# Performance work log

Hardware: AMD Instinct MI355X
Metric: run time of the kernel (lower is better)

The kernel has to match this reference:

```python
import jax, jax.numpy as jnp
import numpy as np

TAU = 2.0      # spikingjelly LIF default membrane time constant
VTH = 1.0      # threshold
SCALE = 0.25
NUM_HEADS = 16
EPS = 1e-5


def lif(x):
    # single-step LIF from rest (v=0, v_reset=0): u = v + (x - v)/tau = x/tau; spike = H(u - vth)
    return (x / TAU >= VTH).astype(x.dtype)


def bn(z, gamma, beta, mean, var):
    # inference-mode BatchNorm1d over channel dim of (TB, C, N)
    inv = gamma / jnp.sqrt(var + EPS)
    return z * inv[:, None] + (beta - mean * inv)[:, None]


def branch(z, w, gamma, beta, mean, var):
    # conv1x1 (pointwise channel mix) -> BN -> LIF
    z = jnp.einsum('oc,bcn->bon', w, z)
    return lif(bn(z, gamma, beta, mean, var))


def setup_inputs() -> dict:
    key = jax.random.key(0)
    ks = jax.random.split(key, 8)
    T, B, C, N = 4, 2, 512, 512
    x = jax.random.normal(ks[0], (T, B, C, N), dtype=jnp.float32)
    y = jax.random.normal(ks[1], (T, B, C, N), dtype=jnp.float32)
    def conv_w(k):
        return jax.random.normal(k, (C, C), dtype=jnp.float32) / np.float32(np.sqrt(C))
    def bn_params(k):
        km, kv = jax.random.split(k)
        gamma = jnp.full((C,), 2.0, dtype=jnp.float32)  # scale so LIF spikes are non-trivially sparse
        beta = jnp.zeros((C,), dtype=jnp.float32)
        mean = 0.1 * jax.random.normal(km, (C,), dtype=jnp.float32)
        var = 0.5 + jax.random.uniform(kv, (C,), dtype=jnp.float32)
        return gamma, beta, mean, var
    q_g, q_b, q_m, q_v = bn_params(ks[2])
    k_g, k_b, k_m, k_v = bn_params(ks[3])
    v_g, v_b, v_m, v_v = bn_params(ks[4])
    p_g, p_b, p_m, p_v = bn_params(ks[5])
    return {
        'x': x, 'y': y,
        'q_w': conv_w(jax.random.fold_in(key, 10)), 'q_g': q_g, 'q_b': q_b, 'q_m': q_m, 'q_v': q_v,
        'k_w': conv_w(jax.random.fold_in(key, 11)), 'k_g': k_g, 'k_b': k_b, 'k_m': k_m, 'k_v': k_v,
        'v_w': conv_w(jax.random.fold_in(key, 12)), 'v_g': v_g, 'v_b': v_b, 'v_m': v_m, 'v_v': v_v,
        'p_w': conv_w(jax.random.fold_in(key, 13)), 'p_g': p_g, 'p_b': p_b, 'p_m': p_m, 'p_v': p_v,
    }


def reference(x, y, q_w, q_g, q_b, q_m, q_v, k_w, k_g, k_b, k_m, k_v,
              v_w, v_g, v_b, v_m, v_v, p_w, p_g, p_b, p_m, p_v):
    T, B, C, N = x.shape
    H = NUM_HEADS
    D = C // H
    xq = x.reshape(T * B, C, N)
    yk = y.reshape(T * B, C, N)
    # q/k/v: conv1x1 + BN + LIF, then split heads: (T,B,C,N) -> (T,B,H,N,D)
    q = branch(xq, q_w, q_g, q_b, q_m, q_v).reshape(T, B, H, D, N).transpose(0, 1, 2, 4, 3)
    k = branch(yk, k_w, k_g, k_b, k_m, k_v).reshape(T, B, H, D, N).transpose(0, 1, 2, 4, 3)
    v = branch(yk, v_w, v_g, v_b, v_m, v_v).reshape(T, B, H, D, N).transpose(0, 1, 2, 4, 3)
    # softmax-free spiking attention: (Q K^T) V * scale
    attn = jnp.einsum('tbhnd,tbhmd->tbhnm', q, k)
    o = jnp.einsum('tbhnm,tbhmd->tbhnd', attn, v) * SCALE
    o = o.transpose(0, 1, 2, 4, 3).reshape(T, B, C, N)  # (T,B,H,D,N) -> (T,B,C,N)
    o = lif(o.reshape(T * B, C, N))
    o = branch(o, p_w, p_g, p_b, p_m, p_v).reshape(T, B, C, N)
    return o
```

## Files before the change

kernel.cpp:

```cpp
#include <hip/hip_runtime.h>
#include <math.h>

#define TBD 8
#define CD  512
#define ND  512
#define PLANE (TBD*CD*ND)
#define WPL   (CD*CD)

typedef unsigned short u16;
typedef unsigned int u32;
typedef _Float16 f16;
typedef __attribute__((ext_vector_type(8))) short bf16x8;
typedef __attribute__((ext_vector_type(8))) _Float16 f16x8;
typedef __attribute__((ext_vector_type(4))) float f32x4;

__device__ __forceinline__ float b2f(u16 u){
  union{u32 i; float f;} x; x.i = ((u32)u) << 16; return x.f;
}
__device__ __forceinline__ u16 f2b(float f){
  u32 u = __builtin_bit_cast(u32, f);
  u += 0x7fffu + ((u >> 16) & 1u);
  return (u16)(u >> 16);
}
__device__ __forceinline__ void async_ld16(const void* g, void* l){
  __builtin_amdgcn_global_load_lds((const __attribute__((address_space(1))) u32*)g,
      (__attribute__((address_space(3))) u32*)l, 16, 0, 0);
}

__global__ __launch_bounds__(256) void prep(
    const float* __restrict__ x, const float* __restrict__ y,
    const float* __restrict__ Qw, const float* __restrict__ Kw,
    const float* __restrict__ Vw, const float* __restrict__ Pw,
    const float* __restrict__ Qg, const float* __restrict__ Qb, const float* __restrict__ Qm, const float* __restrict__ Qv,
    const float* __restrict__ Kg, const float* __restrict__ Kb, const float* __restrict__ Km, const float* __restrict__ Kv,
    const float* __restrict__ Vg, const float* __restrict__ Vb, const float* __restrict__ Vm, const float* __restrict__ Vv,
    const float* __restrict__ Pg, const float* __restrict__ Pb, const float* __restrict__ Pm, const float* __restrict__ Pv,
    u16* __restrict__ wsu, float* __restrict__ ib)
{
  const int bx = blockIdx.x, t = threadIdx.x;
  if (bx < 1024) {
    __shared__ __align__(16) float tl[64][68];
    const int inp = bx >> 9, rem = bx & 511;
    const int tb = rem >> 6, tile = rem & 63;
    const int ct = (tile & 7) << 6, nt = (tile >> 3) << 6;
    const float* xg = inp ? y : x;
    #pragma unroll
    for (int r = 0; r < 4; ++r) {
      const int row = (t >> 4) + (r << 4);
      const int col = (t & 15) << 2;
      *(float4*)&tl[row][col] =
          *(const float4*)(xg + ((size_t)(tb*CD + ct + row))*ND + nt + col);
    }
    __syncthreads();
    const int nl = t >> 2, cb = (t & 3) << 4;
    __align__(16) u16 h[3][16];
    #pragma unroll
    for (int j = 0; j < 16; ++j) {
      const float f = tl[cb + j][nl];
      const u16 a = f2b(f);  const float r1 = f - b2f(a);
      const u16 b = f2b(r1); const float r2 = r1 - b2f(b);
      h[0][j] = a; h[1][j] = b; h[2][j] = f2b(r2);
    }
    u16* base = wsu + (size_t)inp*3*PLANE;
    const size_t rowo = ((size_t)tb*ND + nt + nl)*CD + ct + cb;
    #pragma unroll
    for (int s = 0; s < 3; ++s) {
      *(uint4*)(base + (size_t)s*PLANE + rowo)     = *(uint4*)&h[s][0];
      *(uint4*)(base + (size_t)s*PLANE + rowo + 8) = *(uint4*)&h[s][8];
    }
  } else if (bx < 2048) {
    const int b2 = bx - 1024;
    const int mat = b2 >> 8, rr = b2 & 255;
    const float* Wg = (mat==0)?Qw:(mat==1)?Kw:(mat==2)?Vw:Pw;
    const int row = (rr << 1) + (t >> 7);
    const int col = (t & 127) << 2;
    const float4 w = *(const float4*)(Wg + (size_t)row*CD + col);
    const float f[4] = {w.x, w.y, w.z, w.w};
    __align__(8) u16 h[3][4];
    #pragma unroll
    for (int j = 0; j < 4; ++j) {
      const u16 a = f2b(f[j]);  const float r1 = f[j] - b2f(a);
      const u16 b = f2b(r1);    const float r2 = r1 - b2f(b);
      h[0][j] = a; h[1][j] = b; h[2][j] = f2b(r2);
    }
    u16* base = wsu + (size_t)6*PLANE + (size_t)mat*3*WPL;
    #pragma unroll
    for (int s = 0; s < 3; ++s)
      *(uint2*)(base + (size_t)s*WPL + (size_t)row*CD + col) = *(uint2*)&h[s][0];
  } else {
    const int idx = (bx - 2048)*256 + t;
    const int br = idx >> 9, ch = idx & 511;
    const float* G = (br==0)?Qg:(br==1)?Kg:(br==2)?Vg:Pg;
    const float* B = (br==0)?Qb:(br==1)?Kb:(br==2)?Vb:Pb;
    const float* M = (br==0)?Qm:(br==1)?Km:(br==2)?Vm:Pm;
    const float* V = (br==0)?Qv:(br==1)?Kv:(br==2)?Vv:Pv;
    const float inv = G[ch] / sqrtf(V[ch] + 1e-5f);
    ib[br*1024 + ch]       = inv;
    ib[br*1024 + 512 + ch] = B[ch] - M[ch]*inv;
  }
}

template<int XS>
__global__ __launch_bounds__(256) void gemm_mfma(
    const u16* __restrict__ Ab, const u16* __restrict__ Bbp,
    const float* __restrict__ ibp,
    u16* __restrict__ spk, float* __restrict__ outf)
{
  const int bx  = blockIdx.x;
  const int idx = bx & 511;
  const int br  = bx >> 9;
  const int tb  = idx & 7;
  const int o0  = ((idx >> 3) & 7) << 6;
  const int n0  = (idx >> 6) << 6;
  const int t    = threadIdx.x;
  const int lane = t & 63, wave = t >> 6;

  const u16* A = Ab + (size_t)br*3*WPL;
  const u16* B = Bbp + (size_t)(br ? 3 : 0)*PLANE;
  const float* IB = ibp + br*1024;

  __shared__ __align__(16) u16 smem[2*3*4*512 + 2*XS*4*512];
  u16* Al = smem;
  u16* Bl = smem + 2*3*4*512;

  const int lr = lane >> 2;
  const int lc = ((lane & 3) ^ ((lane >> 3) & 3)) << 3;
  constexpr int TPW = (12 + 4*XS) / 4;

  auto stage = [&](int buf, int c0) {
    #pragma unroll
    for (int j = 0; j < TPW; ++j) {
      const int tix = wave*TPW + j;
      if (tix < 12) {
        const int s = tix >> 2, ot = tix & 3;
        async_ld16(A + (size_t)s*WPL + (size_t)(o0 + (ot<<4) + lr)*CD + c0 + lc,
                   Al + (((buf*3 + s)*4 + ot) << 9) + (lane << 3));
      } else {
        const int k = tix - 12, s = k >> 2, nt = k & 3;
        async_ld16(B + (size_t)s*PLANE + ((size_t)tb*ND + n0 + (nt<<4) + lr)*CD + c0 + lc,
                   Bl + (((buf*XS + s)*4 + nt) << 9) + (lane << 3));
      }
    }
  };

  f32x4 acc[2][2];
  const f32x4 zero = {0.f, 0.f, 0.f, 0.f};
  acc[0][0] = zero; acc[0][1] = zero; acc[1][0] = zero; acc[1][1] = zero;

  const int otb = (wave >> 1) << 1;
  const int ntb = (wave & 1) << 1;
  const int fo = ((lane & 15) << 5) + ((((lane >> 4) ^ ((lane >> 1) & 3)) & 3) << 3);

  stage(0, 0);
  for (int i = 0; i < 16; ++i) {
    const int buf = i & 1;
    __syncthreads();
    if (i < 15) stage(buf ^ 1, (i + 1) << 5);

    bf16x8 Af[3][2], Bf[XS][2];
    #pragma unroll
    for (int s = 0; s < 3; ++s)
      #pragma unroll
      for (int oy = 0; oy < 2; ++oy)
        Af[s][oy] = *(const bf16x8*)(Al + (((buf*3 + s)*4 + otb + oy) << 9) + fo);
    #pragma unroll
    for (int s = 0; s < XS; ++s)
      #pragma unroll
      for (int nx = 0; nx < 2; ++nx)
        Bf[s][nx] = *(const bf16x8*)(Bl + (((buf*XS + s)*4 + ntb + nx) << 9) + fo);

    auto mm = [&](int sa, int sb) {
      #pragma unroll
      for (int oy = 0; oy < 2; ++oy)
        #pragma unroll
        for (int nx = 0; nx < 2; ++nx)
          acc[oy][nx] = __builtin_amdgcn_mfma_f32_16x16x32_bf16(
              Af[sa][oy], Bf[sb][nx], acc[oy][nx], 0, 0, 0);
    };
    if constexpr (XS == 3) {
      mm(0,0); mm(0,1); mm(1,0); mm(1,1); mm(0,2); mm(2,0);
    } else {
      mm(0,0); mm(1,0); mm(2,0);
    }
  }

  const int rbase = (lane >> 4) << 2;
  const int cl = lane & 15;
  #pragma unroll
  for (int oy = 0; oy < 2; ++oy) {
    #pragma unroll
    for (int r = 0; r < 4; ++r) {
      const int ch = o0 + ((otb + oy) << 4) + rbase + r;
      const float inv  = IB[ch];
      const float bias = IB[512 + ch];
      #pragma unroll
      for (int nx = 0; nx < 2; ++nx) {
        const bool sp = (acc[oy][nx][r] * inv + bias >= 2.0f);
        const int n = n0 + ((ntb + nx) << 4) + cl;
        const size_t off = ((size_t)tb*CD + ch)*ND + n;
        if constexpr (XS == 1) outf[off] = sp ? 1.0f : 0.0f;
        else spk[(size_t)br*PLANE + off] = sp ? (u16)0x3C00 : (u16)0;
      }
    }
  }
}

__global__ __launch_bounds__(256) void attn(
    const u16* __restrict__ Qs, const u16* __restrict__ Ks,
    const u16* __restrict__ Vs, u16* __restrict__ S2T)
{
  const int tbh = blockIdx.x >> 2;
  const int n0  = (blockIdx.x & 3) << 7;
  const int t = threadIdx.x, lane = t & 63, wave = t >> 6;
  const int tb = tbh >> 4, h = tbh & 15;

  __shared__ __align__(16) u16 Kt[2*8*512];
  __shared__ __align__(16) u16 Vt[2*8*512];
  __shared__ __align__(16) u16 Qg[8*520];
  __shared__ __align__(16) u16 Gt[4*32*40];
  __shared__ __align__(16) u16 Sb[128*40];

  const u16* Kh = Ks + (size_t)tbh*32*ND;
  const u16* Vh = Vs + (size_t)tbh*32*ND;
  const u16* Qh = Qs + (size_t)tbh*32*ND;

  const int lr = lane >> 2;
  const int lc = ((lane & 3) ^ ((lane >> 3) & 3)) << 3;
  const int fo = ((lane & 15) << 5) + ((((lane >> 4) ^ ((lane >> 1) & 3)) & 3) << 3);

  f32x4 g[2][2];
  const f32x4 zero = {0.f, 0.f, 0.f, 0.f};
  g[0][0] = zero; g[0][1] = zero; g[1][0] = zero; g[1][1] = zero;

  for (int half = 0; half < 2; ++half) {
    if (half) __syncthreads();
    #pragma unroll
    for (int j = 0; j < 8; ++j) {
      const int u = wave*8 + j;
      const int mat = u >> 4, dt = (u >> 3) & 1, kc = u & 7;
      const u16* src = (mat ? Vh : Kh) + (size_t)((dt << 4) + lr)*ND + (half << 8) + (kc << 5) + lc;
      u16* dst = (mat ? Vt : Kt) + (((dt << 3) + kc) << 9) + (lane << 3);
      async_ld16(src, dst);
    }
    if (half == 0) {
      #pragma unroll
      for (int j = 0; j < 2; ++j) {
        const int gq = wave*2 + j;
        async_ld16(Qh + (size_t)((gq << 2) + (lane >> 4))*ND + n0 + ((lane & 15) << 3),
                   Qg + gq*520 + (lane << 3));
      }
    }
    __syncthreads();
    for (int kc = 0; kc < 8; ++kc) {
      const f16* kt = (const f16*)Kt;
      const f16* vt = (const f16*)Vt;
      f16x8 ka0 = *(const f16x8*)(kt + (kc << 9) + fo);
      f16x8 ka1 = *(const f16x8*)(kt + ((8 + kc) << 9) + fo);
      f16x8 vb0 = *(const f16x8*)(vt + (kc << 9) + fo);
      f16x8 vb1 = *(const f16x8*)(vt + ((8 + kc) << 9) + fo);
      g[0][0] = __builtin_amdgcn_mfma_f32_16x16x32_f16(ka0, vb0, g[0][0], 0,0,0);
      g[0][1] = __builtin_amdgcn_mfma_f32_16x16x32_f16(ka0, vb1, g[0][1], 0,0,0);
      g[1][0] = __builtin_amdgcn_mfma_f32_16x16x32_f16(ka1, vb0, g[1][0], 0,0,0);
      g[1][1] = __builtin_amdgcn_mfma_f32_16x16x32_f16(ka1, vb1, g[1][1], 0,0,0);
    }
  }

  f16* myG = (f16*)(Gt + wave*(32*40));
  const int rq = (lane >> 4) << 2, cl = lane & 15;
  #pragma unroll
  for (int d1t = 0; d1t < 2; ++d1t)
    #pragma unroll
    for (int d2t = 0; d2t < 2; ++d2t)
      #pragma unroll
      for (int r = 0; r < 4; ++r) {
        const int d1 = (d1t << 4) + rq + r;
        const int d2 = (d2t << 4) + cl;
        myG[d2*40 + d1] = (f16)g[d1t][d2t][r];
      }
  asm volatile("s_waitcnt lgkmcnt(0)" ::: "memory");

  f32x4 o[2][2];
  o[0][0] = zero; o[0][1] = zero; o[1][0] = zero; o[1][1] = zero;
  const f16* ql = (const f16*)Qg;
  const int kg = lane >> 4, n16 = lane & 15;
  #pragma unroll
  for (int ntl = 0; ntl < 2; ++ntl) {
    const int n0w = ((wave << 1) + ntl) << 4;
    f16x8 qb;
    #pragma unroll
    for (int j = 0; j < 8; ++j)
      qb[j] = ql[(2*kg + (j >> 2))*520 + (j & 3)*128 + n0w + n16];
    #pragma unroll
    for (int dd = 0; dd < 2; ++dd) {
      f16x8 ga = *(const f16x8*)(myG + (((dd << 4) + cl)*40) + (kg << 3));
      o[dd][ntl] = __builtin_amdgcn_mfma_f32_16x16x32_f16(ga, qb, o[dd][ntl], 0,0,0);
    }
  }

  #pragma unroll
  for (int dd = 0; dd < 2; ++dd)
    #pragma unroll
    for (int ntl = 0; ntl < 2; ++ntl)
      #pragma unroll
      for (int r = 0; r < 4; ++r) {
        const int n_local = ((wave*2 + ntl) << 4) + cl;
        const int c_local = (dd << 4) + rq + r;
        Sb[n_local*40 + c_local] = (o[dd][ntl][r] >= 8.0f) ? (u16)0x3F80 : (u16)0;
      }
  asm volatile("s_waitcnt lgkmcnt(0)" ::: "memory");

  const int nr = (wave << 5) + (lane >> 1);
  const int cs = (lane & 1) << 4;
  u16* dst = S2T + ((size_t)tb*ND + n0 + nr)*CD + (h << 5) + cs;
  *(uint4*)dst       = *(uint4*)&Sb[nr*40 + cs];
  *(uint4*)(dst + 8) = *(uint4*)&Sb[nr*40 + cs + 8];
}

extern "C" void kernel_launch(void* const* d_in, const int* in_sizes, int n_in,
                              void* d_out, int out_size, void* d_ws, size_t ws_size,
                              hipStream_t stream)
{
  const float* x  = (const float*)d_in[0];
  const float* y  = (const float*)d_in[1];
  const float* qw = (const float*)d_in[2];
  const float* qg = (const float*)d_in[3];
  const float* qb = (const float*)d_in[4];
  const float* qm = (const float*)d_in[5];
  const float* qv = (const float*)d_in[6];
  const float* kw = (const float*)d_in[7];
  const float* kg = (const float*)d_in[8];
  const float* kb = (const float*)d_in[9];
  const float* km = (const float*)d_in[10];
  const float* kv = (const float*)d_in[11];
  const float* vw = (const float*)d_in[12];
  const float* vg = (const float*)d_in[13];
  const float* vb = (const float*)d_in[14];
  const float* vm = (const float*)d_in[15];
  const float* vv = (const float*)d_in[16];
  const float* pw = (const float*)d_in[17];
  const float* pg = (const float*)d_in[18];
  const float* pb = (const float*)d_in[19];
  const float* pm = (const float*)d_in[20];
  const float* pv = (const float*)d_in[21];

  u16* wsu = (u16*)d_ws;
  u16* Wq   = wsu + (size_t)6*PLANE;
  u16* SPK  = wsu + (size_t)6*PLANE + 12*WPL;
  u16* S2T  = SPK + (size_t)3*PLANE;
  float* ib = (float*)(SPK + (size_t)4*PLANE);

  prep<<<2056, 256, 0, stream>>>(x, y, qw, kw, vw, pw,
      qg, qb, qm, qv, kg, kb, km, kv, vg, vb, vm, vv, pg, pb, pm, pv,
      wsu, ib);

  gemm_mfma<3><<<1536, 256, 0, stream>>>(Wq, wsu, ib, SPK, nullptr);

  attn<<<512, 256, 0, stream>>>(SPK, SPK + (size_t)PLANE, SPK + 2*(size_t)PLANE, S2T);

  gemm_mfma<1><<<512, 256, 0, stream>>>(Wq + (size_t)9*WPL, S2T,
      ib + 3*1024, nullptr, (float*)d_out);
}
```

Measured before the change: 170.8 us.

## Fuse K and V projections sharing Y tile; deepen K-step in output GEMM

The QKV GEMM launch now interleaves blocks. Even blocks compute Q from X, and odd blocks compute K and V together from the same staged Y tile, which halves the loads of Y for those two branches and the block count. The final projection GEMM becomes its own kernel that stages 64-wide K chunks, so it runs 8 iterations instead of 16 and needs fewer barriers. The cost is larger shared memory per block (up to 72KB), which lowers occupancy, and an unbalanced load between Q blocks and K/V blocks.

```diff
diff --git a/kernel.cpp b/kernel.cpp
--- a/kernel.cpp
+++ b/kernel.cpp
@@ -100,108 +100,186 @@
   }
 }
 
-template<int XS>
-__global__ __launch_bounds__(256) void gemm_mfma(
-    const u16* __restrict__ Ab, const u16* __restrict__ Bbp,
-    const float* __restrict__ ibp,
-    u16* __restrict__ spk, float* __restrict__ outf)
+__global__ __launch_bounds__(256) void gemm_qkv(
+    const u16* __restrict__ Wb, const u16* __restrict__ Xs,
+    const u16* __restrict__ Ys, const float* __restrict__ ib,
+    u16* __restrict__ spk)
 {
   const int bx  = blockIdx.x;
-  const int idx = bx & 511;
-  const int br  = bx >> 9;
+  const int idx = bx >> 1;
   const int tb  = idx & 7;
   const int o0  = ((idx >> 3) & 7) << 6;
   const int n0  = (idx >> 6) << 6;
   const int t    = threadIdx.x;
   const int lane = t & 63, wave = t >> 6;
 
-  const u16* A = Ab + (size_t)br*3*WPL;
-  const u16* B = Bbp + (size_t)(br ? 3 : 0)*PLANE;
-  const float* IB = ibp + br*1024;
-
-  __shared__ __align__(16) u16 smem[2*3*4*512 + 2*XS*4*512];
-  u16* Al = smem;
-  u16* Bl = smem + 2*3*4*512;
+  __shared__ __align__(16) u16 smem[2*36*512];
 
   const int lr = lane >> 2;
   const int lc = ((lane & 3) ^ ((lane >> 3) & 3)) << 3;
-  constexpr int TPW = (12 + 4*XS) / 4;
-
-  auto stage = [&](int buf, int c0) {
-    #pragma unroll
-    for (int j = 0; j < TPW; ++j) {
-      const int tix = wave*TPW + j;
-      if (tix < 12) {
-        const int s = tix >> 2, ot = tix & 3;
-        async_ld16(A + (size_t)s*WPL + (size_t)(o0 + (ot<<4) + lr)*CD + c0 + lc,
-                   Al + (((buf*3 + s)*4 + ot) << 9) + (lane << 3));
-      } else {
-        const int k = tix - 12, s = k >> 2, nt = k & 3;
-        async_ld16(B + (size_t)s*PLANE + ((size_t)tb*ND + n0 + (nt<<4) + lr)*CD + c0 + lc,
-                   Bl + (((buf*XS + s)*4 + nt) << 9) + (lane << 3));
-      }
-    }
-  };
-
-  f32x4 acc[2][2];
-  const f32x4 zero = {0.f, 0.f, 0.f, 0.f};
-  acc[0][0] = zero; acc[0][1] = zero; acc[1][0] = zero; acc[1][1] = zero;
-
   const int otb = (wave >> 1) << 1;
   const int ntb = (wave & 1) << 1;
   const int fo = ((lane & 15) << 5) + ((((lane >> 4) ^ ((lane >> 1) & 3)) & 3) << 3);
-
-  stage(0, 0);
-  for (int i = 0; i < 16; ++i) {
-    const int buf = i & 1;
-    __syncthreads();
-    if (i < 15) stage(buf ^ 1, (i + 1) << 5);
-
-    bf16x8 Af[3][2], Bf[XS][2];
-    #pragma unroll
-    for (int s = 0; s < 3; ++s)
-      #pragma unroll
-      for (int oy = 0; oy < 2; ++oy)
-        Af[s][oy] = *(const bf16x8*)(Al + (((buf*3 + s)*4 + otb + oy) << 9) + fo);
-    #pragma unroll
-    for (int s = 0; s < XS; ++s)
-      #pragma unroll
-      for (int nx = 0; nx < 2; ++nx)
-        Bf[s][nx] = *(const bf16x8*)(Bl + (((buf*XS + s)*4 + ntb + nx) << 9) + fo);
-
-    auto mm = [&](int sa, int sb) {
-      #pragma unroll
-      for (int oy = 0; oy < 2; ++oy)
-        #pragma unroll
-        for (int nx = 0; nx < 2; ++nx)
-          acc[oy][nx] = __builtin_amdgcn_mfma_f32_16x16x32_bf16(
-              Af[sa][oy], Bf[sb][nx], acc[oy][nx], 0, 0, 0);
-    };
-    if constexpr (XS == 3) {
-      mm(0,0); mm(0,1); mm(1,0); mm(1,1); mm(0,2); mm(2,0);
-    } else {
-      mm(0,0); mm(1,0); mm(2,0);
-    }
-  }
-
+  const f32x4 zero = {0.f, 0.f, 0.f, 0.f};
   const int rbase = (lane >> 4) << 2;
   const int cl = lane & 15;
-  #pragma unroll
-  for (int oy = 0; oy < 2; ++oy) {
-    #pragma unroll
-    for (int r = 0; r < 4; ++r) {
-      const int ch = o0 + ((otb + oy) << 4) + rbase + r;
-      const float inv  = IB[ch];
-      const float bias = IB[512 + ch];
-      #pragma unroll
-      for (int nx = 0; nx < 2; ++nx) {
-        const bool sp = (acc[oy][nx][r] * inv + bias >= 2.0f);
-        const int n = n0 + ((ntb + nx) << 4) + cl;
-        const size_t off = ((size_t)tb*CD + ch)*ND + n;
-        if constexpr (XS == 1) outf[off] = sp ? 1.0f : 0.0f;
-        else spk[(size_t)br*PLANE + off] = sp ? (u16)0x3C00 : (u16)0;
-      }
-    }
+
+  if (!(bx & 1)) {
+    const u16* A = Wb;
+    const u16* B = Xs;
+    const float* IB = ib;
+    u16* Al = smem;
+    u16* Bl = smem + 2*3*4*512;
+
+    auto stage = [&](int buf, int c0) {
+      #pragma unroll
+      for (int j = 0; j < 6; ++j) {
+        const int tix = wave*6 + j;
+        if (tix < 12) {
+          const int s = tix >> 2, ot = tix & 3;
+          async_ld16(A + (size_t)s*WPL + (size_t)(o0 + (ot<<4) + lr)*CD + c0 + lc,
+                     Al + (((buf*3 + s)*4 + ot) << 9) + (lane << 3));
+        } else {
+          const int k = tix - 12, s = k >> 2, nt = k & 3;
+          async_ld16(B + (size_t)s*PLANE + ((size_t)tb*ND + n0 + (nt<<4) + lr)*CD + c0 + lc,
+                     Bl + (((buf*3 + s)*4 + nt) << 9) + (lane << 3));
+        }
+      }
+    };
+
+    f32x4 acc[2][2];
+    acc[0][0] = zero; acc[0][1] = zero; acc[1][0] = zero; acc[1][1] = zero;
+
+    stage(0, 0);
+    for (int i = 0; i < 16; ++i) {
+      const int buf = i & 1;
+      __syncthreads();
+      if (i < 15) stage(buf ^ 1, (i + 1) << 5);
+
+      bf16x8 Af[3][2], Bf[3][2];
+      #pragma unroll
+      for (int s = 0; s < 3; ++s)
+        #pragma unroll
+        for (int oy = 0; oy < 2; ++oy)
+          Af[s][oy] = *(const bf16x8*)(Al + (((buf*3 + s)*4 + otb + oy) << 9) + fo);
+      #pragma unroll
+      for (int s = 0; s < 3; ++s)
+        #pragma unroll
+        for (int nx = 0; nx < 2; ++nx)
+          Bf[s][nx] = *(const bf16x8*)(Bl + (((buf*3 + s)*4 + ntb + nx) << 9) + fo);
+
+      auto mm = [&](int sa, int sb) {
+        #pragma unroll
+        for (int oy = 0; oy < 2; ++oy)
+          #pragma unroll
+          for (int nx = 0; nx < 2; ++nx)
+            acc[oy][nx] = __builtin_amdgcn_mfma_f32_16x16x32_bf16(
+                Af[sa][oy], Bf[sb][nx], acc[oy][nx], 0, 0, 0);
+      };
+      mm(0,0); mm(0,1); mm(1,0); mm(1,1); mm(0,2); mm(2,0);
+    }
+
+    #pragma unroll
+    for (int oy = 0; oy < 2; ++oy)
+      #pragma unroll
+      for (int r = 0; r < 4; ++r) {
+        const int ch = o0 + ((otb + oy) << 4) + rbase + r;
+        const float inv  = IB[ch];
+        const float bias = IB[512 + ch];
+        #pragma unroll
+        for (int nx = 0; nx < 2; ++nx) {
+          const bool sp = (acc[oy][nx][r] * inv + bias >= 2.0f);
+          const int n = n0 + ((ntb + nx) << 4) + cl;
+          spk[((size_t)tb*CD + ch)*ND + n] = sp ? (u16)0x3C00 : (u16)0;
+        }
+      }
+  } else {
+    const u16* Ak = Wb + (size_t)3*WPL;
+    const u16* Av = Wb + (size_t)6*WPL;
+    const u16* B  = Ys;
+    const float* IBk = ib + 1024;
+    const float* IBv = ib + 2048;
+
+    auto stage = [&](int buf, int c0) {
+      #pragma unroll
+      for (int j = 0; j < 9; ++j) {
+        const int tix = wave*9 + j;
+        const u16* g;
+        if (tix < 12) {
+          const int s = tix >> 2, ot = tix & 3;
+          g = Ak + (size_t)s*WPL + (size_t)(o0 + (ot<<4) + lr)*CD + c0 + lc;
+        } else if (tix < 24) {
+          const int k = tix - 12, s = k >> 2, ot = k & 3;
+          g = Av + (size_t)s*WPL + (size_t)(o0 + (ot<<4) + lr)*CD + c0 + lc;
+        } else {
+          const int k = tix - 24, s = k >> 2, nt = k & 3;
+          g = B + (size_t)s*PLANE + ((size_t)tb*ND + n0 + (nt<<4) + lr)*CD + c0 + lc;
+        }
+        async_ld16(g, smem + (((size_t)buf*36 + tix) << 9) + (lane << 3));
+      }
+    };
+
+    f32x4 ka[2][2], va[2][2];
+    ka[0][0] = zero; ka[0][1] = zero; ka[1][0] = zero; ka[1][1] = zero;
+    va[0][0] = zero; va[0][1] = zero; va[1][0] = zero; va[1][1] = zero;
+
+    stage(0, 0);
+    for (int i = 0; i < 16; ++i) {
+      const int buf = i & 1;
+      __syncthreads();
+      if (i < 15) stage(buf ^ 1, (i + 1) << 5);
+
+      bf16x8 Fk[3][2], Fv[3][2], Fb[3][2];
+      #pragma unroll
+      for (int s = 0; s < 3; ++s)
+        #pragma unroll
+        for (int oy = 0; oy < 2; ++oy) {
+          Fk[s][oy] = *(const bf16x8*)(smem + ((buf*36 + s*4 + otb + oy) << 9) + fo);
+          Fv[s][oy] = *(const bf16x8*)(smem + ((buf*36 + 12 + s*4 + otb + oy) << 9) + fo);
+        }
+      #pragma unroll
+      for (int s = 0; s < 3; ++s)
+        #pragma unroll
+        for (int nx = 0; nx < 2; ++nx)
+          Fb[s][nx] = *(const bf16x8*)(smem + ((buf*36 + 24 + s*4 + ntb + nx) << 9) + fo);
+
+      auto mmk = [&](int sa, int sb) {
+        #pragma unroll
+        for (int oy = 0; oy < 2; ++oy)
+          #pragma unroll
+          for (int nx = 0; nx < 2; ++nx)
+            ka[oy][nx] = __builtin_amdgcn_mfma_f32_16x16x32_bf16(
+                Fk[sa][oy], Fb[sb][nx], ka[oy][nx], 0, 0, 0);
+      };
+      auto mmv = [&](int sa, int sb) {
+        #pragma unroll
+        for (int oy = 0; oy < 2; ++oy)
+          #pragma unroll
+          for (int nx = 0; nx < 2; ++nx)
+            va[oy][nx] = __builtin_amdgcn_mfma_f32_16x16x32_bf16(
+                Fv[sa][oy], Fb[sb][nx], va[oy][nx], 0, 0, 0);
+      };
+      mmk(0,0); mmv(0,0); mmk(0,1); mmv(0,1); mmk(1,0); mmv(1,0);
+      mmk(1,1); mmv(1,1); mmk(0,2); mmv(0,2); mmk(2,0); mmv(2,0);
+    }
+
+    u16* Kout = spk + (size_t)PLANE;
+    u16* Vout = spk + (size_t)2*PLANE;
+    #pragma unroll
+    for (int oy = 0; oy < 2; ++oy)
+      #pragma unroll
+      for (int r = 0; r < 4; ++r) {
+        const int ch = o0 + ((otb + oy) << 4) + rbase + r;
+        const float ivk = IBk[ch], bk = IBk[512 + ch];
+        const float ivv = IBv[ch], bv = IBv[512 + ch];
+        #pragma unroll
+        for (int nx = 0; nx < 2; ++nx) {
+          const int n = n0 + ((ntb + nx) << 4) + cl;
+          const size_t off = ((size_t)tb*CD + ch)*ND + n;
+          Kout[off] = (ka[oy][nx][r] * ivk + bk >= 2.0f) ? (u16)0x3C00 : (u16)0;
+          Vout[off] = (va[oy][nx][r] * ivv + bv >= 2.0f) ? (u16)0x3C00 : (u16)0;
+        }
+      }
   }
 }
 
@@ -314,6 +392,95 @@
   u16* dst = S2T + ((size_t)tb*ND + n0 + nr)*CD + (h << 5) + cs;
   *(uint4*)dst       = *(uint4*)&Sb[nr*40 + cs];
   *(uint4*)(dst + 8) = *(uint4*)&Sb[nr*40 + cs + 8];
+}
+
+__global__ __launch_bounds__(256) void gemm_p(
+    const u16* __restrict__ Ab, const u16* __restrict__ Bb,
+    const float* __restrict__ IB, float* __restrict__ outf)
+{
+  const int idx = blockIdx.x;
+  const int tb  = idx & 7;
+  const int o0  = ((idx >> 3) & 7) << 6;
+  const int n0  = (idx >> 6) << 6;
+  const int t    = threadIdx.x;
+  const int lane = t & 63, wave = t >> 6;
+
+  __shared__ __align__(16) u16 smem[2*32*512];
+
+  const int lr = lane >> 2;
+  const int lc = ((lane & 3) ^ ((lane >> 3) & 3)) << 3;
+  const int otb = (wave >> 1) << 1;
+  const int ntb = (wave & 1) << 1;
+  const int fo = ((lane & 15) << 5) + ((((lane >> 4) ^ ((lane >> 1) & 3)) & 3) << 3);
+
+  auto stage = [&](int buf, int c0) {
+    #pragma unroll
+    for (int j = 0; j < 8; ++j) {
+      const int tix  = wave*8 + j;
+      const int ksub = tix >> 4, slot = tix & 15;
+      const int cc = c0 + (ksub << 5);
+      const u16* g;
+      if (slot < 12) {
+        const int s = slot >> 2, ot = slot & 3;
+        g = Ab + (size_t)s*WPL + (size_t)(o0 + (ot<<4) + lr)*CD + cc + lc;
+      } else {
+        const int nt = slot - 12;
+        g = Bb + ((size_t)tb*ND + n0 + (nt<<4) + lr)*CD + cc + lc;
+      }
+      async_ld16(g, smem + (((size_t)buf*32 + tix) << 9) + (lane << 3));
+    }
+  };
+
+  f32x4 acc[2][2];
+  const f32x4 zero = {0.f, 0.f, 0.f, 0.f};
+  acc[0][0] = zero; acc[0][1] = zero; acc[1][0] = zero; acc[1][1] = zero;
+
+  stage(0, 0);
+  for (int i = 0; i < 8; ++i) {
+    const int buf = i & 1;
+    __syncthreads();
+    if (i < 7) stage(buf ^ 1, (i + 1) << 6);
+
+    #pragma unroll
+    for (int ksub = 0; ksub < 2; ++ksub) {
+      const int base = (buf*32 + ksub*16) << 9;
+      bf16x8 Af[3][2], Bf[2];
+      #pragma unroll
+      for (int s = 0; s < 3; ++s)
+        #pragma unroll
+        for (int oy = 0; oy < 2; ++oy)
+          Af[s][oy] = *(const bf16x8*)(smem + base + ((s*4 + otb + oy) << 9) + fo);
+      #pragma unroll
+      for (int nx = 0; nx < 2; ++nx)
+        Bf[nx] = *(const bf16x8*)(smem + base + ((12 + ntb + nx) << 9) + fo);
+
+      #pragma unroll
+      for (int s = 0; s < 3; ++s)
+        #pragma unroll
+        for (int oy = 0; oy < 2; ++oy)
+          #pragma unroll
+          for (int nx = 0; nx < 2; ++nx)
+            acc[oy][nx] = __builtin_amdgcn_mfma_f32_16x16x32_bf16(
+                Af[s][oy], Bf[nx], acc[oy][nx], 0, 0, 0);
+    }
+  }
+
+  const int rbase = (lane >> 4) << 2;
+  const int cl = lane & 15;
+  #pragma unroll
+  for (int oy = 0; oy < 2; ++oy)
+    #pragma unroll
+    for (int r = 0; r < 4; ++r) {
+      const int ch = o0 + ((otb + oy) << 4) + rbase + r;
+      const float inv  = IB[ch];
+      const float bias = IB[512 + ch];
+      #pragma unroll
+      for (int nx = 0; nx < 2; ++nx) {
+        const bool sp = (acc[oy][nx][r] * inv + bias >= 2.0f);
+        const int n = n0 + ((ntb + nx) << 4) + cl;
+        outf[((size_t)tb*CD + ch)*ND + n] = sp ? 1.0f : 0.0f;
+      }
+    }
 }
 
 extern "C" void kernel_launch(void* const* d_in, const int* in_sizes, int n_in,
@@ -353,10 +520,10 @@
       qg, qb, qm, qv, kg, kb, km, kv, vg, vb, vm, vv, pg, pb, pm, pv,
       wsu, ib);
 
-  gemm_mfma<3><<<1536, 256, 0, stream>>>(Wq, wsu, ib, SPK, nullptr);
+  gemm_qkv<<<1024, 256, 0, stream>>>(Wq, wsu, wsu + (size_t)3*PLANE, ib, SPK);
 
   attn<<<512, 256, 0, stream>>>(SPK, SPK + (size_t)PLANE, SPK + 2*(size_t)PLANE, S2T);
 
-  gemm_mfma<1><<<512, 256, 0, stream>>>(Wq + (size_t)9*WPL, S2T,
-      ib + 3*1024, nullptr, (float*)d_out);
-}
+  gemm_p<<<512, 256, 0, stream>>>(Wq + (size_t)9*WPL, S2T,
+      ib + 3*1024, (float*)d_out);
+}
```

Measured after the change: 172.4 us. Within noise of the previous version (+1.0%).
